# Kernel optimization log

Hardware: AMD Instinct MI355X
Metric: run time of the kernel (lower is better)

Reference implementation:

```python
import jax, jax.numpy as jnp
import numpy as np

D_MODEL = 1024
D_FF = 4096
N_EXP = 8
TOP_K = 2


def _gelu(x):
    # torch F.gelu default is exact (erf) gelu
    return jax.nn.gelu(x, approximate=False)


def setup_inputs() -> dict:
    key = jax.random.key(0)
    ks = jax.random.split(key, 12)
    s = 0.02
    return {
        "x": jax.random.normal(ks[0], (4, 2048, D_MODEL), dtype=jnp.float32),
        "shared_w1": jax.random.normal(ks[1], (D_MODEL, D_FF), dtype=jnp.float32) * s,
        "shared_b1": jnp.zeros((D_FF,), jnp.float32),
        "shared_w2": jax.random.normal(ks[2], (D_FF, D_MODEL), dtype=jnp.float32) * s,
        "shared_b2": jnp.zeros((D_MODEL,), jnp.float32),
        "router_w": jax.random.normal(ks[3], (D_MODEL, N_EXP), dtype=jnp.float32) * s,
        "router_b": jnp.zeros((N_EXP,), jnp.float32),
        "exp_w1": jax.random.normal(ks[4], (N_EXP, D_MODEL, D_FF), dtype=jnp.float32) * s,
        "exp_b1": jnp.zeros((N_EXP, D_FF), jnp.float32),
        "exp_w2": jax.random.normal(ks[5], (N_EXP, D_FF, D_MODEL), dtype=jnp.float32) * s,
        "exp_b2": jnp.zeros((N_EXP, D_MODEL), jnp.float32),
    }


def reference(x, shared_w1, shared_b1, shared_w2, shared_b2,
              router_w, router_b, exp_w1, exp_b1, exp_w2, exp_b2):
    leading = x.shape[:-1]
    d = x.shape[-1]
    xf = x.reshape(-1, d)                                   # [T, d]
    T = xf.shape[0]

    # always-on shared FFN
    h_shared = _gelu(xf @ shared_w1 + shared_b1) @ shared_w2 + shared_b2  # [T, d]

    # router: softmax -> top-k -> renormalize
    logits = xf @ router_w + router_b                       # [T, E]
    routing = jax.nn.softmax(logits, axis=-1)
    sel_w, sel_idx = jax.lax.top_k(routing, TOP_K)          # [T, K]
    sel_w = sel_w / (jnp.sum(sel_w, axis=-1, keepdims=True) + 1e-9)

    # dense combine weights: w[t,e] = sum_k sel_w[t,k] * [sel_idx[t,k]==e]
    combine = jnp.zeros((T, N_EXP), routing.dtype)
    combine = combine.at[jnp.arange(T)[:, None], sel_idx].add(sel_w)

    # specialist residual: sum_e combine[:,e] * FFN_e(x)
    residual = jnp.zeros_like(xf)
    for e in range(N_EXP):                                  # fixed small expert loop
        h = _gelu(xf @ exp_w1[e] + exp_b1[e])               # [T, d_ff]
        y = h @ exp_w2[e] + exp_b2[e]                       # [T, d]
        residual = residual + combine[:, e:e + 1] * y

    out = h_shared + residual
    return out.reshape(*leading, d)
```

## Files before the change

### kernel.cpp

```cpp
#include <hip/hip_runtime.h>
#include <hip/hip_bf16.h>


#define D_MODEL 1024
#define D_FF    4096
#define N_EXP   8
#define T_TOK   8192
#define BK      64

typedef _Float16 half8  __attribute__((ext_vector_type(8)));
typedef _Float16 half4v __attribute__((ext_vector_type(4)));
typedef float    floatx4 __attribute__((ext_vector_type(4)));

__device__ __forceinline__ float gelu_exact(float x) {
  return 0.5f * x * (1.0f + erff(x * 0.70710678118654752f));
}

__device__ __forceinline__ void gld_lds16(const _Float16* g, _Float16* l) {
  __builtin_amdgcn_global_load_lds(
      (const __attribute__((address_space(1))) void*)g,
      (__attribute__((address_space(3))) void*)l, 16, 0, 0);
}

__global__ void convert_f32_f16(const float* __restrict__ src,
                                _Float16* __restrict__ dst, int n4) {
  int i = blockIdx.x * blockDim.x + threadIdx.x;
  if (i >= n4) return;
  float4 v = ((const float4*)src)[i];
  half4v h;
  h[0] = (_Float16)v.x; h[1] = (_Float16)v.y;
  h[2] = (_Float16)v.z; h[3] = (_Float16)v.w;
  ((half4v*)dst)[i] = h;
}

__global__ void transpose_convert9(const float* __restrict__ srcSh,
                                   const float* __restrict__ srcEx,
                                   _Float16* __restrict__ dst, int R, int C) {
  const size_t msz = (size_t)R * C;
  const float* src = (blockIdx.z == 0) ? srcSh : srcEx + msz * (blockIdx.z - 1);
  _Float16* d = dst + msz * blockIdx.z;
  __shared__ float tile[32][33];
  int c0 = blockIdx.x * 32, r0 = blockIdx.y * 32;
  int tx = threadIdx.x, ty = threadIdx.y;
#pragma unroll
  for (int i = 0; i < 4; ++i)
    tile[ty + i * 8][tx] = src[(size_t)(r0 + ty + i * 8) * C + c0 + tx];
  __syncthreads();
#pragma unroll
  for (int i = 0; i < 4; ++i)
    d[(size_t)(c0 + ty + i * 8) * R + r0 + tx] = (_Float16)tile[tx][ty + i * 8];
}

__global__ void router_kernel(const float* __restrict__ x,
                              const float* __restrict__ rw,
                              const float* __restrict__ rb,
                              int* __restrict__ sel_idx,
                              float* __restrict__ sel_w,
                              int* __restrict__ counts) {
  int lane = threadIdx.x & 63;
  int t = blockIdx.x * 4 + (threadIdx.x >> 6);
  const float* xr = x + (size_t)t * D_MODEL;
  float acc[N_EXP];
#pragma unroll
  for (int e = 0; e < N_EXP; ++e) acc[e] = 0.f;
  for (int k = lane; k < D_MODEL; k += 64) {
    float xv = xr[k];
    const float* w = rw + (size_t)k * N_EXP;
#pragma unroll
    for (int e = 0; e < N_EXP; ++e) acc[e] += xv * w[e];
  }
#pragma unroll
  for (int off = 32; off > 0; off >>= 1) {
#pragma unroll
    for (int e = 0; e < N_EXP; ++e)
      acc[e] += __shfl_down(acc[e], off, 64);
  }
  if (lane == 0) {
    float mx = -1e30f;
#pragma unroll
    for (int e = 0; e < N_EXP; ++e) { acc[e] += rb[e]; mx = fmaxf(mx, acc[e]); }
    float p[N_EXP], s = 0.f;
#pragma unroll
    for (int e = 0; e < N_EXP; ++e) { p[e] = expf(acc[e] - mx); s += p[e]; }
    float inv = 1.f / s;
#pragma unroll
    for (int e = 0; e < N_EXP; ++e) p[e] *= inv;
    int i0 = 0; float p0 = p[0];
#pragma unroll
    for (int e = 1; e < N_EXP; ++e) if (p[e] > p0) { p0 = p[e]; i0 = e; }
    int i1 = -1; float p1 = -1.f;
#pragma unroll
    for (int e = 0; e < N_EXP; ++e)
      if (e != i0 && p[e] > p1) { p1 = p[e]; i1 = e; }
    float s2 = p0 + p1 + 1e-9f;
    sel_idx[2 * t] = i0; sel_idx[2 * t + 1] = i1;
    sel_w[2 * t] = p0 / s2; sel_w[2 * t + 1] = p1 / s2;
    atomicAdd(&counts[i0 * 32], 1);
    atomicAdd(&counts[i1 * 32], 1);
  }
}

__global__ void scan_kernel(const int* __restrict__ counts,
                            int* __restrict__ offsets,
                            int* __restrict__ cursor) {
  if (threadIdx.x == 0) {
    int s = 0;
    for (int e = 0; e < N_EXP; ++e) {
      offsets[e] = s; cursor[e * 32] = s; s += counts[e * 32];
    }
    offsets[N_EXP] = s;
  }
}

__global__ void assign_kernel(const int* __restrict__ sel_idx,
                              int* __restrict__ cursor,
                              int* __restrict__ rows,
                              int* __restrict__ inv) {
  int t = blockIdx.x * blockDim.x + threadIdx.x;
  if (t >= T_TOK) return;
#pragma unroll
  for (int k = 0; k < 2; ++k) {
    int e = sel_idx[2 * t + k];
    int pos = atomicAdd(&cursor[e * 32], 1);
    rows[pos] = t;
    inv[2 * t + k] = pos;
  }
}

template <int PHASE>
__global__ __launch_bounds__(512, 2) void gemm_kernel(
    const _Float16* __restrict__ A, const _Float16* __restrict__ Wt,
    const float* __restrict__ biasSh, const float* __restrict__ biasEx,
    _Float16* __restrict__ Hout, float* __restrict__ out,
    float* __restrict__ Yexp, const int* __restrict__ rows,
    const int* __restrict__ counts, const int* __restrict__ offsets) {
  constexpr int K = (PHASE == 1) ? D_MODEL : D_FF;
  constexpr int N = (PHASE == 1) ? D_FF : D_MODEL;
  constexpr int NT = K / BK;
  const int z = blockIdx.z;
  int M = T_TOK, offs = 0;
  if (z > 0) {
    M = counts[(z - 1) * 32];
    offs = offsets[z - 1];
    if ((int)blockIdx.y * 256 >= M) return;
  }
  const int tid = threadIdx.x, lane = tid & 63, wid = tid >> 6;
  const int m0 = blockIdx.y * 256, n0 = blockIdx.x * 256;
  const _Float16* Wz = Wt + (size_t)z * N * K;

  __shared__ __align__(16) _Float16 As[2 * 256 * BK];
  __shared__ __align__(16) _Float16 Bs[2 * 256 * BK];

  const int sub = lane >> 3, pp = lane & 7, g = pp ^ sub;

  const _Float16* aS[4];
  const _Float16* bS[4];
#pragma unroll
  for (int j = 0; j < 4; ++j) {
    int r = m0 + wid * 32 + j * 8 + sub;
    size_t gr;
    if (z == 0) {
      gr = (size_t)r;
    } else {
      int rc = r < M ? r : M - 1;
      if constexpr (PHASE == 1) gr = (size_t)rows[offs + rc];
      else                      gr = (size_t)(T_TOK + offs + rc);
    }
    aS[j] = A + gr * K + g * 8;
    bS[j] = Wz + (size_t)(n0 + wid * 32 + j * 8 + sub) * K + g * 8;
  }

#pragma unroll
  for (int j = 0; j < 4; ++j) {
    gld_lds16(aS[j], As + (wid * 4 + j) * 512); aS[j] += BK;
  }
#pragma unroll
  for (int j = 0; j < 4; ++j) {
    gld_lds16(bS[j], Bs + (wid * 4 + j) * 512); bS[j] += BK;
  }

  floatx4 acc[8][4] = {};
  const int wm = wid >> 2, wn = wid & 3;
  const int lr = lane & 15, qd = lane >> 4;
  const int xm = lr & 7;

#pragma unroll 2
  for (int t = 0; t < NT; ++t) {
    _Float16* Ac = As + (t & 1) * (256 * BK);
    _Float16* Bc = Bs + (t & 1) * (256 * BK);
    _Float16* An = As + ((t & 1) ^ 1) * (256 * BK);
    _Float16* Bn = Bs + ((t & 1) ^ 1) * (256 * BK);
    if (t + 1 < NT) {
#pragma unroll
      for (int j = 0; j < 4; ++j) {
        gld_lds16(aS[j], An + (wid * 4 + j) * 512); aS[j] += BK;
      }
      asm volatile("s_waitcnt vmcnt(4)" ::: "memory");
    } else {
      asm volatile("s_waitcnt vmcnt(0)" ::: "memory");
    }
    __builtin_amdgcn_s_barrier();
    asm volatile("" ::: "memory");
    __builtin_amdgcn_sched_barrier(0);
#pragma unroll
    for (int ks = 0; ks < 2; ++ks) {
      half8 af[8], bf[4];
      const int slot = (ks * 4 + qd) ^ xm;
#pragma unroll
      for (int mi = 0; mi < 8; ++mi)
        af[mi] = *(const half8*)(Ac + (wm * 128 + mi * 16 + lr) * BK + slot * 8);
#pragma unroll
      for (int ni = 0; ni < 4; ++ni)
        bf[ni] = *(const half8*)(Bc + (wn * 64 + ni * 16 + lr) * BK + slot * 8);
      __builtin_amdgcn_s_setprio(1);
#pragma unroll
      for (int mi = 0; mi < 8; ++mi)
#pragma unroll
        for (int ni = 0; ni < 4; ++ni)
          acc[mi][ni] = __builtin_amdgcn_mfma_f32_16x16x32_f16(
              af[mi], bf[ni], acc[mi][ni], 0, 0, 0);
      __builtin_amdgcn_s_setprio(0);
      if (ks == 0 && t + 1 < NT) {
#pragma unroll
        for (int j = 0; j < 4; ++j) {
          gld_lds16(bS[j], Bn + (wid * 4 + j) * 512); bS[j] += BK;
        }
      }
    }
    asm volatile("s_waitcnt lgkmcnt(0)" ::: "memory");
    __builtin_amdgcn_sched_barrier(0);
    __builtin_amdgcn_s_barrier();
  }

  const float* be = (z == 0) ? biasSh : biasEx + (size_t)(z - 1) * N;
#pragma unroll
  for (int mi = 0; mi < 8; ++mi) {
#pragma unroll
    for (int ni = 0; ni < 4; ++ni) {
      floatx4 v = acc[mi][ni];
#pragma unroll
      for (int r4 = 0; r4 < 4; ++r4) {
        const int lrow = m0 + wm * 128 + mi * 16 + qd * 4 + r4;
        const int col = n0 + wn * 64 + ni * 16 + lr;
        const float val = v[r4] + be[col];
        if constexpr (PHASE == 1) {
          if (z == 0) {
            Hout[(size_t)lrow * N + col] = (_Float16)gelu_exact(val);
          } else if (lrow < M) {
            Hout[(size_t)(T_TOK + offs + lrow) * N + col] =
                (_Float16)gelu_exact(val);
          }
        } else {
          if (z == 0) {
            out[(size_t)lrow * N + col] = val;
          } else if (lrow < M) {
            Yexp[(size_t)(offs + lrow) * N + col] = val;
          }
        }
      }
    }
  }
}

__global__ void combine_kernel(float* __restrict__ out,
                               const float* __restrict__ Yexp,
                               const int* __restrict__ inv,
                               const float* __restrict__ selw) {
  const int t = blockIdx.x;
  const int c = threadIdx.x * 4;
  const int p0 = inv[2 * t], p1 = inv[2 * t + 1];
  const float w0 = selw[2 * t], w1 = selw[2 * t + 1];
  float4 o = *(float4*)(out + (size_t)t * D_MODEL + c);
  const float4 a = *(const float4*)(Yexp + (size_t)p0 * D_MODEL + c);
  const float4 b = *(const float4*)(Yexp + (size_t)p1 * D_MODEL + c);
  o.x += w0 * a.x + w1 * b.x;
  o.y += w0 * a.y + w1 * b.y;
  o.z += w0 * a.z + w1 * b.z;
  o.w += w0 * a.w + w1 * b.w;
  *(float4*)(out + (size_t)t * D_MODEL + c) = o;
}

extern "C" void kernel_launch(void* const* d_in, const int* in_sizes, int n_in,
                              void* d_out, int out_size, void* d_ws,
                              size_t ws_size, hipStream_t stream) {
  const float* x   = (const float*)d_in[0];
  const float* sw1 = (const float*)d_in[1];
  const float* sb1 = (const float*)d_in[2];
  const float* sw2 = (const float*)d_in[3];
  const float* sb2 = (const float*)d_in[4];
  const float* rw  = (const float*)d_in[5];
  const float* rb  = (const float*)d_in[6];
  const float* ew1 = (const float*)d_in[7];
  const float* eb1 = (const float*)d_in[8];
  const float* ew2 = (const float*)d_in[9];
  const float* eb2 = (const float*)d_in[10];
  float* out = (float*)d_out;

  char* ws = (char*)d_ws;
  size_t off = 0;
  auto alloc = [&](size_t bytes) {
    void* p = ws + off;
    off += (bytes + 255) & ~(size_t)255;
    return p;
  };
  _Float16* xb  = (_Float16*)alloc((size_t)T_TOK * D_MODEL * 2);
  _Float16* w2t = (_Float16*)alloc((size_t)9 * D_MODEL * D_FF * 2);
  _Float16* H   = (_Float16*)alloc((size_t)3 * T_TOK * D_FF * 2);
  _Float16* w1t = (_Float16*)alloc((size_t)9 * D_FF * D_MODEL * 2);
  float* Yexp   = (float*)w1t;
  int*   sel_idx = (int*)alloc((size_t)T_TOK * 2 * 4);
  float* sel_w   = (float*)alloc((size_t)T_TOK * 2 * 4);
  int*   rows    = (int*)alloc((size_t)2 * T_TOK * 4);
  int*   inv     = (int*)alloc((size_t)2 * T_TOK * 4);
  int*   counts  = (int*)alloc(N_EXP * 32 * 4);
  int*   offsets = (int*)alloc(16 * 4);
  int*   cursor  = (int*)alloc(N_EXP * 32 * 4);
  (void)ws_size; (void)in_sizes; (void)n_in; (void)out_size;

  hipMemsetAsync(counts, 0, N_EXP * 32 * 4, stream);

  convert_f32_f16<<<(T_TOK * D_MODEL / 4 + 255) / 256, 256, 0, stream>>>(
      x, xb, T_TOK * D_MODEL / 4);
  dim3 tb(32, 8);
  transpose_convert9<<<dim3(D_FF / 32, D_MODEL / 32, 9), tb, 0, stream>>>(
      sw1, ew1, w1t, D_MODEL, D_FF);
  transpose_convert9<<<dim3(D_MODEL / 32, D_FF / 32, 9), tb, 0, stream>>>(
      sw2, ew2, w2t, D_FF, D_MODEL);

  router_kernel<<<T_TOK / 4, 256, 0, stream>>>(x, rw, rb, sel_idx, sel_w, counts);
  scan_kernel<<<1, 64, 0, stream>>>(counts, offsets, cursor);
  assign_kernel<<<T_TOK / 256, 256, 0, stream>>>(sel_idx, cursor, rows, inv);

  gemm_kernel<1><<<dim3(D_FF / 256, T_TOK / 256, 9), 512, 0, stream>>>(
      xb, w1t, sb1, eb1, H, nullptr, nullptr, rows, counts, offsets);
  gemm_kernel<2><<<dim3(D_MODEL / 256, T_TOK / 256, 9), 512, 0, stream>>>(
      H, w2t, sb2, eb2, nullptr, out, Yexp, rows, counts, offsets);

  combine_kernel<<<T_TOK, 256, 0, stream>>>(out, Yexp, inv, sel_w);
}
```

Before: 1.214 ms.

## Switch GEMM mainloop to 4-stage BK=32 LDS pipeline with one barrier per step

```diff
diff --git a/kernel.cpp b/kernel.cpp
--- a/kernel.cpp
+++ b/kernel.cpp
@@ -6,7 +6,6 @@
 #define D_FF    4096
 #define N_EXP   8
 #define T_TOK   8192
-#define BK      64
 
 typedef _Float16 half8  __attribute__((ext_vector_type(8)));
 typedef _Float16 half4v __attribute__((ext_vector_type(4)));
@@ -136,7 +135,9 @@
     const int* __restrict__ counts, const int* __restrict__ offsets) {
   constexpr int K = (PHASE == 1) ? D_MODEL : D_FF;
   constexpr int N = (PHASE == 1) ? D_FF : D_MODEL;
-  constexpr int NT = K / BK;
+  constexpr int BK2 = 32;
+  constexpr int NT = K / BK2;
+  constexpr int TSZ = 256 * BK2;
   const int z = blockIdx.z;
   int M = T_TOK, offs = 0;
   if (z > 0) {
@@ -148,87 +149,80 @@
   const int m0 = blockIdx.y * 256, n0 = blockIdx.x * 256;
   const _Float16* Wz = Wt + (size_t)z * N * K;
 
-  __shared__ __align__(16) _Float16 As[2 * 256 * BK];
-  __shared__ __align__(16) _Float16 Bs[2 * 256 * BK];
-
-  const int sub = lane >> 3, pp = lane & 7, g = pp ^ sub;
-
-  const _Float16* aS[4];
-  const _Float16* bS[4];
-#pragma unroll
-  for (int j = 0; j < 4; ++j) {
-    int r = m0 + wid * 32 + j * 8 + sub;
-    size_t gr;
+  __shared__ __align__(16) _Float16 As[4 * TSZ];
+  __shared__ __align__(16) _Float16 Bs[4 * TSZ];
+
+  const int sub = lane >> 2;
+  const int g = (lane & 3) ^ (sub & 3);
+
+  size_t grA0, grA1;
+  {
+    int r0 = m0 + wid * 32 + 0 * 16 + sub;
+    int r1 = m0 + wid * 32 + 1 * 16 + sub;
     if (z == 0) {
-      gr = (size_t)r;
+      grA0 = (size_t)r0; grA1 = (size_t)r1;
     } else {
-      int rc = r < M ? r : M - 1;
-      if constexpr (PHASE == 1) gr = (size_t)rows[offs + rc];
-      else                      gr = (size_t)(T_TOK + offs + rc);
+      int c0 = r0 < M ? r0 : M - 1;
+      int c1 = r1 < M ? r1 : M - 1;
+      if constexpr (PHASE == 1) {
+        grA0 = (size_t)rows[offs + c0];
+        grA1 = (size_t)rows[offs + c1];
+      } else {
+        grA0 = (size_t)(T_TOK + offs + c0);
+        grA1 = (size_t)(T_TOK + offs + c1);
+      }
     }
-    aS[j] = A + gr * K + g * 8;
-    bS[j] = Wz + (size_t)(n0 + wid * 32 + j * 8 + sub) * K + g * 8;
-  }
-
-#pragma unroll
-  for (int j = 0; j < 4; ++j) {
-    gld_lds16(aS[j], As + (wid * 4 + j) * 512); aS[j] += BK;
-  }
-#pragma unroll
-  for (int j = 0; j < 4; ++j) {
-    gld_lds16(bS[j], Bs + (wid * 4 + j) * 512); bS[j] += BK;
-  }
+  }
+  const _Float16* aS0 = A + grA0 * K + g * 8;
+  const _Float16* aS1 = A + grA1 * K + g * 8;
+  const _Float16* bS0 = Wz + (size_t)(n0 + wid * 32 + 0 * 16 + sub) * K + g * 8;
+  const _Float16* bS1 = Wz + (size_t)(n0 + wid * 32 + 1 * 16 + sub) * K + g * 8;
+  const int ldsOff = wid * 32 * BK2;
+
+  auto STAGE = [&](int b) {
+    _Float16* Ad = As + b * TSZ + ldsOff;
+    _Float16* Bd = Bs + b * TSZ + ldsOff;
+    gld_lds16(aS0, Ad);             aS0 += BK2;
+    gld_lds16(aS1, Ad + 16 * BK2);  aS1 += BK2;
+    gld_lds16(bS0, Bd);             bS0 += BK2;
+    gld_lds16(bS1, Bd + 16 * BK2);  bS1 += BK2;
+  };
 
   floatx4 acc[8][4] = {};
   const int wm = wid >> 2, wn = wid & 3;
   const int lr = lane & 15, qd = lane >> 4;
-  const int xm = lr & 7;
-
-#pragma unroll 2
+  const int rslot = (qd ^ (lr & 3)) * 8;
+
+  STAGE(0); STAGE(1); STAGE(2);
+  asm volatile("s_waitcnt vmcnt(8)" ::: "memory");
+  __builtin_amdgcn_s_barrier();
+
   for (int t = 0; t < NT; ++t) {
-    _Float16* Ac = As + (t & 1) * (256 * BK);
-    _Float16* Bc = Bs + (t & 1) * (256 * BK);
-    _Float16* An = As + ((t & 1) ^ 1) * (256 * BK);
-    _Float16* Bn = Bs + ((t & 1) ^ 1) * (256 * BK);
-    if (t + 1 < NT) {
-#pragma unroll
-      for (int j = 0; j < 4; ++j) {
-        gld_lds16(aS[j], An + (wid * 4 + j) * 512); aS[j] += BK;
-      }
+    if (t + 3 < NT) STAGE((t + 3) & 3);
+    const _Float16* Ac = As + (t & 3) * TSZ;
+    const _Float16* Bc = Bs + (t & 3) * TSZ;
+    half8 af[8], bf[4];
+#pragma unroll
+    for (int mi = 0; mi < 8; ++mi)
+      af[mi] = *(const half8*)(Ac + (wm * 128 + mi * 16 + lr) * BK2 + rslot);
+#pragma unroll
+    for (int ni = 0; ni < 4; ++ni)
+      bf[ni] = *(const half8*)(Bc + (wn * 64 + ni * 16 + lr) * BK2 + rslot);
+    __builtin_amdgcn_s_setprio(1);
+#pragma unroll
+    for (int mi = 0; mi < 8; ++mi)
+#pragma unroll
+      for (int ni = 0; ni < 4; ++ni)
+        acc[mi][ni] = __builtin_amdgcn_mfma_f32_16x16x32_f16(
+            af[mi], bf[ni], acc[mi][ni], 0, 0, 0);
+    __builtin_amdgcn_s_setprio(0);
+    if (t + 3 < NT) {
+      asm volatile("s_waitcnt vmcnt(8)" ::: "memory");
+    } else if (t + 3 == NT) {
       asm volatile("s_waitcnt vmcnt(4)" ::: "memory");
     } else {
       asm volatile("s_waitcnt vmcnt(0)" ::: "memory");
     }
-    __builtin_amdgcn_s_barrier();
-    asm volatile("" ::: "memory");
-    __builtin_amdgcn_sched_barrier(0);
-#pragma unroll
-    for (int ks = 0; ks < 2; ++ks) {
-      half8 af[8], bf[4];
-      const int slot = (ks * 4 + qd) ^ xm;
-#pragma unroll
-      for (int mi = 0; mi < 8; ++mi)
-        af[mi] = *(const half8*)(Ac + (wm * 128 + mi * 16 + lr) * BK + slot * 8);
-#pragma unroll
-      for (int ni = 0; ni < 4; ++ni)
-        bf[ni] = *(const half8*)(Bc + (wn * 64 + ni * 16 + lr) * BK + slot * 8);
-      __builtin_amdgcn_s_setprio(1);
-#pragma unroll
-      for (int mi = 0; mi < 8; ++mi)
-#pragma unroll
-        for (int ni = 0; ni < 4; ++ni)
-          acc[mi][ni] = __builtin_amdgcn_mfma_f32_16x16x32_f16(
-              af[mi], bf[ni], acc[mi][ni], 0, 0, 0);
-      __builtin_amdgcn_s_setprio(0);
-      if (ks == 0 && t + 1 < NT) {
-#pragma unroll
-        for (int j = 0; j < 4; ++j) {
-          gld_lds16(bS[j], Bn + (wid * 4 + j) * 512); bS[j] += BK;
-        }
-      }
-    }
-    asm volatile("s_waitcnt lgkmcnt(0)" ::: "memory");
-    __builtin_amdgcn_sched_barrier(0);
     __builtin_amdgcn_s_barrier();
   }
 
```

Result: slower. 1.345 ms (+10.8%).
